# Performance work log

Measured on AMD Instinct MI355X. Metric: run time of the kernel, lower is better.

## Reference

```python
import jax, jax.numpy as jnp
import numpy as np

RADIUS = 3.0
NSAMPLE = 16


def _projection(pc, theta, phi, r=1.0):
    # pc: (B,N,3); theta,phi: (M,) -> (B,M,N,2)
    sint, cost = jnp.sin(theta), jnp.cos(theta)
    sinp, cosp = jnp.sin(phi), jnp.cos(phi)
    U = jnp.stack([-sint, cost, jnp.zeros_like(theta)], -1)            # (M,3)
    V = jnp.stack([cost * sinp, sint * sinp, cosp], -1)                # (M,3)
    basis = jnp.stack([U, V], -1)                                      # (M,3,2)
    center = jnp.stack([cost * cosp, sint * cosp, sinp], -1) * r       # (M,3)
    return jnp.einsum('bmnd,mdk->bmnk', pc[:, None, :, :] - center[None, :, None, :], basis)


def _point2mask(coords, feats, valid, H, W):
    # coords (G,N,2), feats (G,N,C), valid (G,N) bool mask of real (non-pad) points
    G, N, _ = coords.shape
    p = jnp.array([H, W], jnp.float32)
    cmax = coords.max(1, keepdims=True)
    cmin = coords.min(1, keepdims=True)
    center = jax.lax.stop_gradient((cmax + cmin) / 2)
    scale = jax.lax.stop_gradient(jnp.maximum(cmax - cmin, 1e-5) / 2)
    coords = ((coords - center) / scale + 1.0) * 0.8 * p / 2 + 0.1 * p
    gx, gy = jnp.meshgrid(jnp.arange(H), jnp.arange(W), indexing='ij')
    samples = jnp.stack([gx, gy], -1).reshape(-1, 2).astype(jnp.float32)  # (S,2)
    pts = jnp.sort(feats, -1)[..., -2:]                                   # (G,N,2) top-2 scores
    # 2D ball query: (G,S,N) squared distances grid-cell -> point
    d2 = jnp.sum((samples[None, :, None, :] - coords[:, None, :, :]) ** 2, -1)
    within = (d2 < RADIUS ** 2) & valid[:, None, :]
    # first NSAMPLE in-ball point indices per query (smallest index first)
    keyi = jnp.where(within, jnp.arange(N, dtype=jnp.int32), jnp.int32(N))
    negv, _ = jax.lax.top_k(-keyi, NSAMPLE)
    idx = -negv                                                           # (G,S,NSAMPLE)
    slot_ok = idx < N
    idx = jnp.where(slot_ok, idx, 0)
    grouped = pts[jnp.arange(G)[:, None, None], idx]                      # (G,S,NSAMPLE,2)
    grouped = jnp.where(slot_ok[..., None], grouped, 0.0)
    occ = jnp.sum(grouped != 0.0, axis=2)                                 # (G,S,2)
    occ = jnp.where(occ == 0, 1, occ)
    nf = jnp.sum(grouped, axis=2) / occ                                   # occupancy-weighted mean
    nf = jax.nn.softmax(nf, -1)
    empty = (nf[..., 0] == nf[..., 1])[..., None]
    nf = jnp.where(empty, jnp.array([1.0, 0.0], nf.dtype), nf)            # masked_scatter [1,0]
    return nf.reshape(G, H, W, 2)


def reference(xyz, features, boxes, theta, phi, res):
    H = W = res
    B, N, _ = xyz.shape
    K = boxes.shape[1]
    M = theta.shape[0]
    pc_coords = _projection(xyz, theta, phi, r=1.0)                       # (B,M,N,2)

    def per_sample(pc, feats, coords_mv, boxpool):
        # crop each box; emulate crop+mean-pad with a fixed-N mask (pads are mean values,
        # excluded from the ball query via `valid`, exactly as points_num does in torch)
        valid = jnp.all(pc[None] <= boxpool[:, None, 3:], -1) & \
                jnp.all(pc[None] >= boxpool[:, None, :3], -1)             # (K,N)
        vf = valid.astype(feats.dtype)
        cnt = vf.sum(1)                                                    # (K,)
        mean_c = jnp.einsum('mnd,kn->kmd', coords_mv, vf) / cnt[:, None, None]
        mean_f = (vf @ feats) / cnt[:, None]
        coords_box = jnp.where(valid[:, None, :, None], coords_mv[None], mean_c[:, :, None, :])  # (K,M,N,2)
        feats_box = jnp.where(valid[:, :, None], feats[None], mean_f[:, None, :])                # (K,N,C)
        g_coords = coords_box.reshape(K * M, N, 2)
        g_feats = jnp.repeat(feats_box, M, axis=0)                         # repeat_interleave over views
        g_valid = jnp.repeat(valid, M, axis=0)
        mask = _point2mask(g_coords, g_feats, g_valid, H, W)               # (K*M,H,W,2)
        return jnp.repeat(mask[..., 1:], 3, -1) * 255.0                    # (K*M,H,W,3)

    masks = jax.vmap(per_sample)(xyz, features, pc_coords, boxes)          # (B,K*M,H,W,3)
    return masks.reshape(B * K * M, H, W, 3).transpose(0, 3, 1, 2)


def setup_inputs() -> dict:
    key = jax.random.key(0)
    ks = jax.random.split(key, 6)
    B, N, C, K, M = 1, 4096, 20, 6, 3
    xyz = jax.random.normal(ks[0], (B, N, 3), jnp.float32)
    features = jax.random.normal(ks[1], (B, N, C), jnp.float32)
    ctr = jax.random.uniform(ks[2], (B, K, 3), minval=-0.5, maxval=0.5)
    half = jax.random.uniform(ks[3], (B, K, 3), minval=0.6, maxval=1.2)
    boxes = jnp.concatenate([ctr - half, ctr + half], -1)                  # (B,K,6) non-empty boxes
    theta = jax.random.uniform(ks[4], (M,), minval=0.0, maxval=2 * np.pi)
    phi = jax.random.uniform(ks[5], (M,), minval=-np.pi / 3, maxval=np.pi / 3)
    return {"xyz": xyz, "features": features, "boxes": boxes, "theta": theta, "phi": phi, "res": 48}
```

## Files before the change

### kernel.cpp

```cpp
#include <hip/hip_runtime.h>
#include <math.h>

#pragma clang fp contract(off)

#define NPTS 4096
#define NC   20
#define NK   6
#define NM   3
#define NG   (NK*NM)
#define RES  48
#define NPIX (RES*RES)
#define NSAMP 16
#define TS   8
#define TPG  (RES/TS)
#define NTIL (TPG*TPG)
#define NSL  8
#define SLPTS (NPTS/NSL)
#define BT   (NSL*64)
#define PPT  (NPTS/BT)

__global__ void k_pre(const float* __restrict__ feats, const float* __restrict__ theta,
                      const float* __restrict__ phi,
                      float* __restrict__ trig, float2* __restrict__ pt2) {
  int b = blockIdx.x, t = threadIdx.x;
  if (b == 16) {
    if (t < 12) {
      int m = t >> 2, w = t & 3;
      double a = (w < 2) ? (double)theta[m] : (double)phi[m];
      double r = (w & 1) ? cos(a) : sin(a);
      trig[m*4 + w] = (float)r;
    }
    return;
  }
  int n = b*256 + t;
  const float4* f4 = (const float4*)(feats + n*NC);
  float m1 = -INFINITY, m2 = -INFINITY;
  #pragma unroll
  for (int q = 0; q < 5; ++q) {
    float4 f = f4[q];
    float e[4] = {f.x, f.y, f.z, f.w};
    #pragma unroll
    for (int j = 0; j < 4; ++j) {
      float v = e[j];
      if (v > m1) { m2 = m1; m1 = v; }
      else if (v > m2) { m2 = v; }
    }
  }
  pt2[n] = make_float2(m2, m1);
}

__global__ void __launch_bounds__(BT, 4) k_mega(const float* __restrict__ xyz,
    const float* __restrict__ boxes, const float* __restrict__ trig,
    const float2* __restrict__ pt2, float* __restrict__ out) {
  int tile = blockIdx.x, g = blockIdx.y;
  int k = g / NM, m = g - k * NM;
  int t = threadIdx.x, w = t >> 6, lane = t & 63;

  __shared__ float2 spts[NPTS];
  __shared__ unsigned short sidx[NSL][64][NSAMP+1];
  __shared__ unsigned char scnt[NSL][64];
  __shared__ float cred[NSL][4];
  __shared__ float csh[4];

  float st = trig[4*m+0], ct = trig[4*m+1], sp = trig[4*m+2], cp = trig[4*m+3];
  float cxc = ct*cp, cyc = st*cp, czc = sp;
  float b0 = boxes[k*6+0], b1 = boxes[k*6+1], b2 = boxes[k*6+2];
  float b3 = boxes[k*6+3], b4 = boxes[k*6+4], b5 = boxes[k*6+5];

  float uu[PPT], vv[PPT];
  unsigned vbits = 0;
  float mn0 = INFINITY, mn1 = INFINITY, mx0 = -INFINITY, mx1 = -INFINITY;
  #pragma unroll
  for (int i = 0; i < PPT; ++i) {
    int n = t + i*BT;
    float x = xyz[n*3+0], y = xyz[n*3+1], z = xyz[n*3+2];
    float dx = x - cxc, dy = y - cyc, dz = z - czc;
    float u = dx*(-st) + dy*ct;
    float v = (dx*(ct*sp) + dy*(st*sp)) + dz*cp;
    uu[i] = u; vv[i] = v;
    bool val = (x >= b0) && (y >= b1) && (z >= b2) &&
               (x <= b3) && (y <= b4) && (z <= b5);
    if (val) {
      vbits |= (1u << i);
      mn0 = fminf(mn0,u); mx0 = fmaxf(mx0,u);
      mn1 = fminf(mn1,v); mx1 = fmaxf(mx1,v);
    }
  }
  #pragma unroll
  for (int off = 1; off < 64; off <<= 1) {
    mn0 = fminf(mn0, __shfl_xor(mn0, off)); mx0 = fmaxf(mx0, __shfl_xor(mx0, off));
    mn1 = fminf(mn1, __shfl_xor(mn1, off)); mx1 = fmaxf(mx1, __shfl_xor(mx1, off));
  }
  if (lane == 0) { cred[w][0]=mn0; cred[w][1]=mn1; cred[w][2]=mx0; cred[w][3]=mx1; }
  __syncthreads();
  if (t == 0) {
    float a0=cred[0][0], a1=cred[0][1], a2=cred[0][2], a3=cred[0][3];
    #pragma unroll
    for (int ww = 1; ww < NSL; ++ww) {
      a0 = fminf(a0, cred[ww][0]); a1 = fminf(a1, cred[ww][1]);
      a2 = fmaxf(a2, cred[ww][2]); a3 = fmaxf(a3, cred[ww][3]);
    }
    csh[0] = (a2 + a0) / 2.0f;
    csh[1] = (a3 + a1) / 2.0f;
    csh[2] = fmaxf(a2 - a0, 1e-5f) / 2.0f;
    csh[3] = fmaxf(a3 - a1, 1e-5f) / 2.0f;
  }
  __syncthreads();

  {
    float c0=csh[0], c1=csh[1], s0=csh[2], s1=csh[3];
    #pragma unroll
    for (int i = 0; i < PPT; ++i) {
      int n = t + i*BT;
      float2 o;
      if ((vbits >> i) & 1u) {
        float u = uu[i], v = vv[i];
        u = (u - c0) / s0; u = u + 1.0f; u = u * 0.8f; u = u * (float)RES; u = u / 2.0f; u = u + 0.1f*(float)RES;
        v = (v - c1) / s1; v = v + 1.0f; v = v * 0.8f; v = v * (float)RES; v = v / 2.0f; v = v + 0.1f*(float)RES;
        o = make_float2(u, v);
      } else {
        o = make_float2(1e30f, 1e30f);
      }
      spts[n] = o;
    }
  }
  __syncthreads();

  int ti = tile / TPG, tj = tile - (tile / TPG) * TPG;
  float si = (float)(ti*TS + (lane >> 3));
  float sj = (float)(tj*TS + (lane & 7));
  float lo0 = (float)(ti*TS) - 3.0f, hi0 = (float)(ti*TS + TS - 1) + 3.0f;
  float lo1 = (float)(tj*TS) - 3.0f, hi1 = (float)(tj*TS + TS - 1) + 3.0f;

  int cnt = 0;
  int base0 = w * SLPTS;
  for (int c = 0; c < SLPTS/64; ++c) {
    int base = base0 + c*64;
    float2 pl = spts[base + lane];
    bool cand = (pl.x >= lo0) && (pl.x <= hi0) && (pl.y >= lo1) && (pl.y <= hi1);
    unsigned long long msk = __ballot(cand);
    while (msk) {
      int jj = __builtin_ctzll(msk);
      msk &= msk - 1ull;
      int n = base + jj;
      float2 pq = spts[n];
      float dx = si - pq.x, dy = sj - pq.y;
      float d2 = dx*dx + dy*dy;
      if (d2 < 9.0f && cnt < NSAMP) {
        sidx[w][lane][cnt] = (unsigned short)n;
        ++cnt;
      }
    }
    if (__all(cnt >= NSAMP)) break;
  }
  scnt[w][lane] = (unsigned char)cnt;
  __syncthreads();

  int p = t >> 3, q = t & 7;
  int tt[NSL+1]; tt[0] = 0;
  #pragma unroll
  for (int ww = 0; ww < NSL; ++ww) {
    int s2 = tt[ww] + (int)scnt[ww][p];
    tt[ww+1] = s2 > NSAMP ? NSAMP : s2;
  }
  float sum0 = 0.f, sum1 = 0.f, occ0 = 0.f, occ1 = 0.f;
  for (int r = q; r < tt[NSL]; r += 8) {
    int wsel = 0, i2 = r;
    #pragma unroll
    for (int ww = 1; ww < NSL; ++ww) if (r >= tt[ww]) { wsel = ww; i2 = r - tt[ww]; }
    int n = sidx[wsel][p][i2];
    float2 f = pt2[n];
    sum0 += f.x; sum1 += f.y;
    occ0 += (f.x != 0.f) ? 1.f : 0.f;
    occ1 += (f.y != 0.f) ? 1.f : 0.f;
  }
  sum0 += __shfl_xor(sum0,1); sum0 += __shfl_xor(sum0,2); sum0 += __shfl_xor(sum0,4);
  sum1 += __shfl_xor(sum1,1); sum1 += __shfl_xor(sum1,2); sum1 += __shfl_xor(sum1,4);
  occ0 += __shfl_xor(occ0,1); occ0 += __shfl_xor(occ0,2); occ0 += __shfl_xor(occ0,4);
  occ1 += __shfl_xor(occ1,1); occ1 += __shfl_xor(occ1,2); occ1 += __shfl_xor(occ1,4);

  if (q == 0) {
    float o0 = (occ0 == 0.f) ? 1.f : occ0;
    float o1 = (occ1 == 0.f) ? 1.f : occ1;
    float nf0 = sum0 / o0, nf1 = sum1 / o1;
    float mxv = fmaxf(nf0, nf1);
    float e0 = expf(nf0 - mxv), e1 = expf(nf1 - mxv);
    float a1 = e1 / (e0 + e1);
    float val = (nf0 == nf1) ? 0.f : a1 * 255.f;
    int pi = ti*TS + (p >> 3), pj = tj*TS + (p & 7);
    int base2 = g*3*NPIX + pi*RES + pj;
    out[base2] = val;
    out[base2 + NPIX] = val;
    out[base2 + 2*NPIX] = val;
  }
}

extern "C" void kernel_launch(void* const* d_in, const int* in_sizes, int n_in,
                              void* d_out, int out_size, void* d_ws, size_t ws_size,
                              hipStream_t stream) {
  const float* xyz   = (const float*)d_in[0];
  const float* feats = (const float*)d_in[1];
  const float* boxes = (const float*)d_in[2];
  const float* theta = (const float*)d_in[3];
  const float* phi   = (const float*)d_in[4];
  float* out = (float*)d_out;

  char* ws = (char*)d_ws;
  float*  trig = (float*)ws;
  float2* pt2  = (float2*)(ws + 64);

  k_pre<<<17, 256, 0, stream>>>(feats, theta, phi, trig, pt2);
  k_mega<<<dim3(NTIL, NG), BT, 0, stream>>>(xyz, boxes, trig, pt2, out);
}
```

Measured before the change: 25.02 us.

## Fuse preprocessing into single kernel and keep projected points in registers

Removes the separate preprocessing kernel. Each block now computes the trig values itself, and the top-2 feature scores are computed on demand for only the gathered neighbor indices. Each wave now projects exactly the point slice it later scans, so the shared-memory point array and one barrier go away; candidate coordinates are broadcast with cross-lane shuffles, four at a time. This saves a kernel launch and shared-memory traffic. In exchange, every block redundantly recomputes trig and per-neighbor top-2 over 20 features, and the launch-bounds occupancy hint is dropped.

```diff
diff --git a/kernel.cpp b/kernel.cpp
--- a/kernel.cpp
+++ b/kernel.cpp
@@ -17,67 +17,44 @@
 #define NSL  8
 #define SLPTS (NPTS/NSL)
 #define BT   (NSL*64)
-#define PPT  (NPTS/BT)
-
-__global__ void k_pre(const float* __restrict__ feats, const float* __restrict__ theta,
-                      const float* __restrict__ phi,
-                      float* __restrict__ trig, float2* __restrict__ pt2) {
-  int b = blockIdx.x, t = threadIdx.x;
-  if (b == 16) {
-    if (t < 12) {
-      int m = t >> 2, w = t & 3;
-      double a = (w < 2) ? (double)theta[m] : (double)phi[m];
-      double r = (w & 1) ? cos(a) : sin(a);
-      trig[m*4 + w] = (float)r;
-    }
-    return;
-  }
-  int n = b*256 + t;
-  const float4* f4 = (const float4*)(feats + n*NC);
-  float m1 = -INFINITY, m2 = -INFINITY;
-  #pragma unroll
-  for (int q = 0; q < 5; ++q) {
-    float4 f = f4[q];
-    float e[4] = {f.x, f.y, f.z, f.w};
-    #pragma unroll
-    for (int j = 0; j < 4; ++j) {
-      float v = e[j];
-      if (v > m1) { m2 = m1; m1 = v; }
-      else if (v > m2) { m2 = v; }
-    }
-  }
-  pt2[n] = make_float2(m2, m1);
-}
-
-__global__ void __launch_bounds__(BT, 4) k_mega(const float* __restrict__ xyz,
-    const float* __restrict__ boxes, const float* __restrict__ trig,
-    const float2* __restrict__ pt2, float* __restrict__ out) {
+#define CPS  (SLPTS/64)
+
+__global__ void __launch_bounds__(BT) k_all(const float* __restrict__ xyz,
+    const float* __restrict__ feats, const float* __restrict__ boxes,
+    const float* __restrict__ theta, const float* __restrict__ phi,
+    float* __restrict__ out) {
   int tile = blockIdx.x, g = blockIdx.y;
   int k = g / NM, m = g - k * NM;
   int t = threadIdx.x, w = t >> 6, lane = t & 63;
 
-  __shared__ float2 spts[NPTS];
+  __shared__ float trig_s[4];
   __shared__ unsigned short sidx[NSL][64][NSAMP+1];
   __shared__ unsigned char scnt[NSL][64];
   __shared__ float cred[NSL][4];
   __shared__ float csh[4];
 
-  float st = trig[4*m+0], ct = trig[4*m+1], sp = trig[4*m+2], cp = trig[4*m+3];
+  if (t < 4) {
+    double a = (t < 2) ? (double)theta[m] : (double)phi[m];
+    double r = (t & 1) ? cos(a) : sin(a);
+    trig_s[t] = (float)r;
+  }
+  __syncthreads();
+  float st = trig_s[0], ct = trig_s[1], sp = trig_s[2], cp = trig_s[3];
   float cxc = ct*cp, cyc = st*cp, czc = sp;
   float b0 = boxes[k*6+0], b1 = boxes[k*6+1], b2 = boxes[k*6+2];
   float b3 = boxes[k*6+3], b4 = boxes[k*6+4], b5 = boxes[k*6+5];
 
-  float uu[PPT], vv[PPT];
+  float pu[CPS], pv[CPS];
   unsigned vbits = 0;
   float mn0 = INFINITY, mn1 = INFINITY, mx0 = -INFINITY, mx1 = -INFINITY;
   #pragma unroll
-  for (int i = 0; i < PPT; ++i) {
-    int n = t + i*BT;
+  for (int i = 0; i < CPS; ++i) {
+    int n = w*SLPTS + i*64 + lane;
     float x = xyz[n*3+0], y = xyz[n*3+1], z = xyz[n*3+2];
     float dx = x - cxc, dy = y - cyc, dz = z - czc;
     float u = dx*(-st) + dy*ct;
     float v = (dx*(ct*sp) + dy*(st*sp)) + dz*cp;
-    uu[i] = u; vv[i] = v;
+    pu[i] = u; pv[i] = v;
     bool val = (x >= b0) && (y >= b1) && (z >= b2) &&
                (x <= b3) && (y <= b4) && (z <= b5);
     if (val) {
@@ -110,21 +87,17 @@
   {
     float c0=csh[0], c1=csh[1], s0=csh[2], s1=csh[3];
     #pragma unroll
-    for (int i = 0; i < PPT; ++i) {
-      int n = t + i*BT;
-      float2 o;
+    for (int i = 0; i < CPS; ++i) {
       if ((vbits >> i) & 1u) {
-        float u = uu[i], v = vv[i];
+        float u = pu[i], v = pv[i];
         u = (u - c0) / s0; u = u + 1.0f; u = u * 0.8f; u = u * (float)RES; u = u / 2.0f; u = u + 0.1f*(float)RES;
         v = (v - c1) / s1; v = v + 1.0f; v = v * 0.8f; v = v * (float)RES; v = v / 2.0f; v = v + 0.1f*(float)RES;
-        o = make_float2(u, v);
+        pu[i] = u; pv[i] = v;
       } else {
-        o = make_float2(1e30f, 1e30f);
+        pu[i] = 1e30f; pv[i] = 1e30f;
       }
-      spts[n] = o;
-    }
-  }
-  __syncthreads();
+    }
+  }
 
   int ti = tile / TPG, tj = tile - (tile / TPG) * TPG;
   float si = (float)(ti*TS + (lane >> 3));
@@ -133,26 +106,37 @@
   float lo1 = (float)(tj*TS) - 3.0f, hi1 = (float)(tj*TS + TS - 1) + 3.0f;
 
   int cnt = 0;
-  int base0 = w * SLPTS;
-  for (int c = 0; c < SLPTS/64; ++c) {
-    int base = base0 + c*64;
-    float2 pl = spts[base + lane];
-    bool cand = (pl.x >= lo0) && (pl.x <= hi0) && (pl.y >= lo1) && (pl.y <= hi1);
-    unsigned long long msk = __ballot(cand);
-    while (msk) {
-      int jj = __builtin_ctzll(msk);
-      msk &= msk - 1ull;
-      int n = base + jj;
-      float2 pq = spts[n];
-      float dx = si - pq.x, dy = sj - pq.y;
-      float d2 = dx*dx + dy*dy;
-      if (d2 < 9.0f && cnt < NSAMP) {
-        sidx[w][lane][cnt] = (unsigned short)n;
-        ++cnt;
-      }
-    }
-    if (__all(cnt >= NSAMP)) break;
-  }
+  bool done = false;
+  #define CHUNK(c)                                                              \
+  if (!done) {                                                                  \
+    float px = pu[c], py = pv[c];                                               \
+    bool cand = (px >= lo0) && (px <= hi0) && (py >= lo1) && (py <= hi1);       \
+    unsigned long long msk = __ballot(cand);                                    \
+    int base = w*SLPTS + (c)*64;                                                \
+    while (msk) {                                                               \
+      int j0 = __builtin_ctzll(msk); msk &= msk - 1ull;                         \
+      int j1 = j0, j2 = j0, j3 = j0, have = 1;                                  \
+      if (msk) { j1 = __builtin_ctzll(msk); msk &= msk - 1ull; have = 2;        \
+        if (msk) { j2 = __builtin_ctzll(msk); msk &= msk - 1ull; have = 3;      \
+          if (msk) { j3 = __builtin_ctzll(msk); msk &= msk - 1ull; have = 4; }}}\
+      float x0 = __shfl(px, j0), y0 = __shfl(py, j0);                           \
+      float x1 = __shfl(px, j1), y1 = __shfl(py, j1);                           \
+      float x2 = __shfl(px, j2), y2 = __shfl(py, j2);                           \
+      float x3 = __shfl(px, j3), y3 = __shfl(py, j3);                           \
+      float dx, dy, d2;                                                         \
+      dx = si - x0; dy = sj - y0; d2 = dx*dx + dy*dy;                           \
+      if (d2 < 9.0f && cnt < NSAMP) { sidx[w][lane][cnt] = (unsigned short)(base + j0); ++cnt; } \
+      if (have > 1) { dx = si - x1; dy = sj - y1; d2 = dx*dx + dy*dy;           \
+        if (d2 < 9.0f && cnt < NSAMP) { sidx[w][lane][cnt] = (unsigned short)(base + j1); ++cnt; } } \
+      if (have > 2) { dx = si - x2; dy = sj - y2; d2 = dx*dx + dy*dy;           \
+        if (d2 < 9.0f && cnt < NSAMP) { sidx[w][lane][cnt] = (unsigned short)(base + j2); ++cnt; } } \
+      if (have > 3) { dx = si - x3; dy = sj - y3; d2 = dx*dx + dy*dy;           \
+        if (d2 < 9.0f && cnt < NSAMP) { sidx[w][lane][cnt] = (unsigned short)(base + j3); ++cnt; } } \
+    }                                                                           \
+    if (__all(cnt >= NSAMP)) done = true;                                       \
+  }
+  CHUNK(0) CHUNK(1) CHUNK(2) CHUNK(3) CHUNK(4) CHUNK(5) CHUNK(6) CHUNK(7)
+  #undef CHUNK
   scnt[w][lane] = (unsigned char)cnt;
   __syncthreads();
 
@@ -169,10 +153,20 @@
     #pragma unroll
     for (int ww = 1; ww < NSL; ++ww) if (r >= tt[ww]) { wsel = ww; i2 = r - tt[ww]; }
     int n = sidx[wsel][p][i2];
-    float2 f = pt2[n];
-    sum0 += f.x; sum1 += f.y;
-    occ0 += (f.x != 0.f) ? 1.f : 0.f;
-    occ1 += (f.y != 0.f) ? 1.f : 0.f;
+    const float4* f4 = (const float4*)(feats + n*NC);
+    float m1 = -INFINITY, m2 = -INFINITY;
+    #pragma unroll
+    for (int qq = 0; qq < 5; ++qq) {
+      float4 f = f4[qq];
+      float e0 = f.x, e1 = f.y, e2 = f.z, e3 = f.w;
+      if (e0 > m1) { m2 = m1; m1 = e0; } else if (e0 > m2) { m2 = e0; }
+      if (e1 > m1) { m2 = m1; m1 = e1; } else if (e1 > m2) { m2 = e1; }
+      if (e2 > m1) { m2 = m1; m1 = e2; } else if (e2 > m2) { m2 = e2; }
+      if (e3 > m1) { m2 = m1; m1 = e3; } else if (e3 > m2) { m2 = e3; }
+    }
+    sum0 += m2; sum1 += m1;
+    occ0 += (m2 != 0.f) ? 1.f : 0.f;
+    occ1 += (m1 != 0.f) ? 1.f : 0.f;
   }
   sum0 += __shfl_xor(sum0,1); sum0 += __shfl_xor(sum0,2); sum0 += __shfl_xor(sum0,4);
   sum1 += __shfl_xor(sum1,1); sum1 += __shfl_xor(sum1,2); sum1 += __shfl_xor(sum1,4);
@@ -204,11 +198,7 @@
   const float* theta = (const float*)d_in[3];
   const float* phi   = (const float*)d_in[4];
   float* out = (float*)d_out;
-
-  char* ws = (char*)d_ws;
-  float*  trig = (float*)ws;
-  float2* pt2  = (float2*)(ws + 64);
-
-  k_pre<<<17, 256, 0, stream>>>(feats, theta, phi, trig, pt2);
-  k_mega<<<dim3(NTIL, NG), BT, 0, stream>>>(xyz, boxes, trig, pt2, out);
+  (void)d_ws; (void)ws_size;
+
+  k_all<<<dim3(NTIL, NG), BT, 0, stream>>>(xyz, feats, boxes, theta, phi, out);
 }
```

Measured after the change: 24.91 us. About the same (-0.4%).
